# Kernel tuning notes

Hardware: AMD Instinct MI355X
Metric: run time of the kernel (lower is better)

The kernel has to match this reference:

```python
import jax, jax.numpy as jnp
import numpy as np

B, N, C, K, D, H = 4, 16384, 256, 16, 4, 512
EPS = 1e-5


def setup_inputs() -> dict:
    key = jax.random.key(0)
    ks = jax.random.split(key, 16)
    s = 0.05  # weight scale
    inp = {
        "x": jax.random.normal(ks[0], (B, N, C), jnp.float32),
        "knn": jax.random.randint(ks[1], (B, N, K), 0, N, jnp.int32),
        "lfp_w": jax.random.normal(ks[2], (D, C, C), jnp.float32) * s,
        "lfp_bn_w": jax.random.uniform(ks[3], (D, C), jnp.float32),
        "lfp_bn_b": jax.random.normal(ks[4], (D, C), jnp.float32) * s,
        "mlp0_w1": jax.random.normal(ks[5], (C, H), jnp.float32) * s,
        "mlp0_b1": jax.random.normal(ks[6], (H,), jnp.float32) * s,
        "mlp0_w2": jax.random.normal(ks[7], (H, C), jnp.float32) * s,
        "mlp0_bn_w": jax.random.uniform(ks[8], (C,), jnp.float32),
        "mlp0_bn_b": jax.random.normal(ks[9], (C,), jnp.float32) * s,
        "mlps_w1": jax.random.normal(ks[10], (D // 2, C, H), jnp.float32) * s,
        "mlps_b1": jax.random.normal(ks[11], (D // 2, H), jnp.float32) * s,
        "mlps_w2": jax.random.normal(ks[12], (D // 2, H, C), jnp.float32) * s,
        "mlps_bn_w": jax.random.uniform(ks[13], (D // 2, C), jnp.float32),
        "mlps_bn_b": jax.random.normal(ks[14], (D // 2, C), jnp.float32) * s,
    }
    return inp


def _bn(y, w, b):
    # BatchNorm1d over flattened (B*N) rows, biased variance, train-mode stats
    m = y.mean(axis=(0, 1))
    v = ((y - m) ** 2).mean(axis=(0, 1))
    return (y - m) * jax.lax.rsqrt(v + EPS) * w + b


def _mlp(y, w1, b1, w2, bw, bb):
    h = jax.nn.gelu(jnp.einsum("bnc,ch->bnh", y, w1) + b1, approximate=False)
    return _bn(jnp.einsum("bnh,hc->bnc", h, w2), bw, bb)


def _lfp(y, knn, w, bw, bb):
    p = jnp.einsum("bnc,cd->bnd", y, w)               # linear proj, no bias
    nb = jax.vmap(lambda pb, kb: pb[kb])(p, knn)      # [B,N,K,C] neighbor gather
    return _bn(nb.max(axis=2) - p, bw, bb)            # max over knn minus self


def reference(x, knn, lfp_w, lfp_bn_w, lfp_bn_b,
              mlp0_w1, mlp0_b1, mlp0_w2, mlp0_bn_w, mlp0_bn_b,
              mlps_w1, mlps_b1, mlps_w2, mlps_bn_w, mlps_bn_b):
    # Block.forward (eval: drop_path = identity)
    x = x + _mlp(x, mlp0_w1, mlp0_b1, mlp0_w2, mlp0_bn_w, mlp0_bn_b)
    depth = lfp_w.shape[0]
    for i in range(depth):
        x = x + _lfp(x, knn, lfp_w[i], lfp_bn_w[i], lfp_bn_b[i])
        if i % 2 == 1:
            j = i // 2
            x = x + _mlp(x, mlps_w1[j], mlps_b1[j], mlps_w2[j],
                         mlps_bn_w[j], mlps_bn_b[j])
    return x
```

## Files before the change

### kernel.cpp

```cpp
#include <hip/hip_runtime.h>
#include <hip/hip_bf16.h>

#define M_TOTAL 65536
#define NPTS    16384
#define CDIM    256
#define KNN     16
#define HDIM    512
#define CSTR    136

typedef __bf16 bf16x8 __attribute__((ext_vector_type(8)));
typedef float  f32x4  __attribute__((ext_vector_type(4)));

__device__ inline float b2f(unsigned u) {
    union { unsigned v; float f; } x; x.v = u << 16; return x.f;
}
__device__ inline unsigned short f2b(float f) {
    union { float f; unsigned u; } x; x.f = f;
    unsigned r = x.u + 0x7fffu + ((x.u >> 16) & 1u);
    return (unsigned short)(r >> 16);
}
__device__ inline void gload_lds16(const void* g, void* l) {
    __builtin_amdgcn_global_load_lds(
        (const __attribute__((address_space(1))) unsigned*)g,
        (__attribute__((address_space(3))) unsigned*)l, 16, 0, 0);
}
__device__ inline float gelu_tanh(float u) {
    const float t = u * (0.7978845608f + 0.0356774081f * u * u);
    const float e = __expf(2.f * t);
    const float th = 1.f - 2.f * __builtin_amdgcn_rcpf(e + 1.f);
    return 0.5f * u * (1.f + th);
}

template<int MODE>
__global__ __launch_bounds__(256) void gemm_nt(
    const short* __restrict__ A, const short* __restrict__ BT,
    short* __restrict__ outB,
    const float* __restrict__ bias, float2* __restrict__ partials,
    int N, int K)
{
    __shared__ short a_lds[128 * 32];
    __shared__ short b_lds[128 * 32];
    __shared__ short c_lds[128 * CSTR];
    __shared__ float s_sum[128], s_sq[128];

    const int tid = threadIdx.x;
    const int nx = gridDim.x, nwg = nx * gridDim.y;
    const int bid = blockIdx.y * nx + blockIdx.x;
    const int lid = (bid & 7) * (nwg >> 3) + (bid >> 3);
    const int m0 = (lid / nx) * 128, n0 = (lid % nx) * 128;

    const int w = tid >> 6, l = tid & 63;
    const int wm = w >> 1, wn = w & 1;

    if (MODE == 2 && tid < 128) { s_sum[tid] = 0.f; s_sq[tid] = 0.f; }

    f32x4 acc[4][4] = {};

    const int lrow = l & 15, lk = (l >> 4) * 8;
    const int q0 = 2 * w, q1 = 2 * w + 1;
    const int gr = l >> 2, gc = (l & 3) * 8;
    const size_t arow0 = (size_t)(m0 + q0 * 16 + gr) * K + gc;
    const size_t arow1 = (size_t)(m0 + q1 * 16 + gr) * K + gc;
    const size_t brow0 = (size_t)(n0 + q0 * 16 + gr) * K + gc;
    const size_t brow1 = (size_t)(n0 + q1 * 16 + gr) * K + gc;

    const int nkt = K >> 5;
    for (int kt = 0; kt < nkt; ++kt) {
        const int k0 = kt << 5;
        if (kt) __syncthreads();
        gload_lds16(A  + arow0 + k0, a_lds + q0 * 512);
        gload_lds16(A  + arow1 + k0, a_lds + q1 * 512);
        gload_lds16(BT + brow0 + k0, b_lds + q0 * 512);
        gload_lds16(BT + brow1 + k0, b_lds + q1 * 512);
        __syncthreads();

        bf16x8 af[4], bfr[4];
#pragma unroll
        for (int i = 0; i < 4; ++i)
            af[i] = *(const bf16x8*)(a_lds + (wm * 64 + i * 16 + lrow) * 32 + lk);
#pragma unroll
        for (int j = 0; j < 4; ++j)
            bfr[j] = *(const bf16x8*)(b_lds + (wn * 64 + j * 16 + lrow) * 32 + lk);
#pragma unroll
        for (int i = 0; i < 4; ++i)
#pragma unroll
            for (int j = 0; j < 4; ++j)
                acc[i][j] = __builtin_amdgcn_mfma_f32_16x16x32_bf16(
                    af[i], bfr[j], acc[i][j], 0, 0, 0);
    }

    const int lq = l >> 4;
#pragma unroll
    for (int j = 0; j < 4; ++j) {
        const int cl  = wn * 64 + j * 16 + lrow;
        const float bsv = (MODE == 1) ? bias[n0 + cl] : 0.f;
        float psum = 0.f, psq = 0.f;
#pragma unroll
        for (int i = 0; i < 4; ++i) {
#pragma unroll
            for (int r = 0; r < 4; ++r) {
                const int row = wm * 64 + i * 16 + lq * 4 + r;
                float v = acc[i][j][r];
                if (MODE == 1) v = gelu_tanh(v + bsv);
                c_lds[row * CSTR + cl] = (short)f2b(v);
                if (MODE == 2) { psum += v; psq += v * v; }
            }
        }
        if (MODE == 2) {
            atomicAdd(&s_sum[cl], psum);
            atomicAdd(&s_sq[cl], psq);
        }
    }
    __syncthreads();
#pragma unroll
    for (int it = 0; it < 8; ++it) {
        const int idx = it * 256 + tid;
        const int row = idx >> 4, ch = idx & 15;
        const uint4 vv = *(const uint4*)&c_lds[row * CSTR + ch * 8];
        *(uint4*)&outB[(size_t)(m0 + row) * N + n0 + ch * 8] = vv;
    }
    if (MODE == 2 && tid < 128)
        partials[(size_t)(m0 >> 7) * N + n0 + tid] =
            make_float2(s_sum[tid], s_sq[tid]);
}

__global__ __launch_bounds__(256) void gather_max(
    const short* __restrict__ p, const int* __restrict__ knn,
    short* __restrict__ yout, float2* __restrict__ partials, int pass)
{
    __shared__ float s_sum[128], s_sq[128];
    const int tid = threadIdx.x, w = tid >> 6, l = tid & 63;
    if (tid < 128) { s_sum[tid] = 0.f; s_sq[tid] = 0.f; }
    __syncthreads();

    const int xcd = blockIdx.x & 7, hi = blockIdx.x >> 3;
    const int gblk = (xcd >> 1) * 512 + (hi << 1) + (xcd & 1);

    const int sub = l >> 5;
    const int cl  = (l & 31) * 4;
    const int coff = pass * 128 + cl;

    float sa0 = 0, sa1 = 0, sa2 = 0, sa3 = 0;
    float qa0 = 0, qa1 = 0, qa2 = 0, qa3 = 0;
    for (int it = 0; it < 4; ++it) {
        const size_t g = (size_t)gblk * 32 + w * 8 + it * 2 + sub;
        const int b = (int)(g >> 14);
        const int n = (int)(g & (NPTS - 1));
        const int4* kp4 = (const int4*)(knn + ((size_t)b * NPTS + n) * KNN);
        int idxs[16];
        {
            const int4 i0 = kp4[0], i1 = kp4[1], i2 = kp4[2], i3 = kp4[3];
            idxs[0]=i0.x; idxs[1]=i0.y; idxs[2]=i0.z; idxs[3]=i0.w;
            idxs[4]=i1.x; idxs[5]=i1.y; idxs[6]=i1.z; idxs[7]=i1.w;
            idxs[8]=i2.x; idxs[9]=i2.y; idxs[10]=i2.z; idxs[11]=i2.w;
            idxs[12]=i3.x; idxs[13]=i3.y; idxs[14]=i3.z; idxs[15]=i3.w;
        }
        const size_t pbase = (size_t)b * NPTS * CDIM + coff;
        float mx0 = -1e30f, mx1 = -1e30f, mx2 = -1e30f, mx3 = -1e30f;
#pragma unroll
        for (int k = 0; k < KNN; ++k) {
            const uint2 v = *(const uint2*)(p + pbase + (size_t)idxs[k] * CDIM);
            mx0 = fmaxf(mx0, b2f(v.x & 0xffffu));
            mx1 = fmaxf(mx1, b2f(v.x >> 16));
            mx2 = fmaxf(mx2, b2f(v.y & 0xffffu));
            mx3 = fmaxf(mx3, b2f(v.y >> 16));
        }
        const uint2 sv = *(const uint2*)(p + g * CDIM + coff);
        const float t0 = mx0 - b2f(sv.x & 0xffffu);
        const float t1 = mx1 - b2f(sv.x >> 16);
        const float t2 = mx2 - b2f(sv.y & 0xffffu);
        const float t3 = mx3 - b2f(sv.y >> 16);
        uint2 pk;
        pk.x = (unsigned)f2b(t0) | ((unsigned)f2b(t1) << 16);
        pk.y = (unsigned)f2b(t2) | ((unsigned)f2b(t3) << 16);
        *(uint2*)(yout + g * CDIM + coff) = pk;
        sa0 += t0; sa1 += t1; sa2 += t2; sa3 += t3;
        qa0 += t0 * t0; qa1 += t1 * t1; qa2 += t2 * t2; qa3 += t3 * t3;
    }
    atomicAdd(&s_sum[cl + 0], sa0); atomicAdd(&s_sq[cl + 0], qa0);
    atomicAdd(&s_sum[cl + 1], sa1); atomicAdd(&s_sq[cl + 1], qa1);
    atomicAdd(&s_sum[cl + 2], sa2); atomicAdd(&s_sq[cl + 2], qa2);
    atomicAdd(&s_sum[cl + 3], sa3); atomicAdd(&s_sq[cl + 3], qa3);
    __syncthreads();
    if (tid < 128)
        partials[(size_t)gblk * CDIM + pass * 128 + tid] =
            make_float2(s_sum[tid], s_sq[tid]);
}

__global__ __launch_bounds__(256) void reduce_stats(
    const float2* __restrict__ partials, int nblk,
    const float* __restrict__ bnw, const float* __restrict__ bnb,
    float2* __restrict__ scsh)
{
    __shared__ float ss[4], qq[4];
    const int c = blockIdx.x;
    const int tid = threadIdx.x, w = tid >> 6, l = tid & 63;
    float s = 0.f, q = 0.f;
    for (int rb = tid; rb < nblk; rb += 256) {
        const float2 v = partials[(size_t)rb * CDIM + c];
        s += v.x; q += v.y;
    }
#pragma unroll
    for (int off = 32; off > 0; off >>= 1) {
        s += __shfl_down(s, off);
        q += __shfl_down(q, off);
    }
    if (l == 0) { ss[w] = s; qq[w] = q; }
    __syncthreads();
    if (tid == 0) {
        const float S = ss[0] + ss[1] + ss[2] + ss[3];
        const float Q = qq[0] + qq[1] + qq[2] + qq[3];
        const float invM = 1.f / 65536.f;
        const float mean = S * invM;
        const float var  = Q * invM - mean * mean;
        const float istd = rsqrtf(var + 1e-5f);
        const float sc   = bnw[c] * istd;
        scsh[c] = make_float2(sc, bnb[c] - mean * sc);
    }
}

__global__ __launch_bounds__(256) void bn_residual(
    const short* __restrict__ y, const float* __restrict__ resid,
    const float2* __restrict__ scsh,
    float* __restrict__ xout, short* __restrict__ xbout)
{
    const size_t t = (size_t)blockIdx.x * 256 + threadIdx.x;
    const uint2 yv = ((const uint2*)y)[t];
    const float4 rv = ((const float4*)resid)[t];
    const int c0 = (int)((t * 4) & (CDIM - 1));
    const float2 s0 = scsh[c0], s1 = scsh[c0 + 1], s2 = scsh[c0 + 2], s3 = scsh[c0 + 3];
    const float o0 = rv.x + b2f(yv.x & 0xffffu) * s0.x + s0.y;
    const float o1 = rv.y + b2f(yv.x >> 16)     * s1.x + s1.y;
    const float o2 = rv.z + b2f(yv.y & 0xffffu) * s2.x + s2.y;
    const float o3 = rv.w + b2f(yv.y >> 16)     * s3.x + s3.y;
    ((float4*)xout)[t] = make_float4(o0, o1, o2, o3);
    if (xbout) {
        uint2 pk;
        pk.x = (unsigned)f2b(o0) | ((unsigned)f2b(o1) << 16);
        pk.y = (unsigned)f2b(o2) | ((unsigned)f2b(o3) << 16);
        ((uint2*)xbout)[t] = pk;
    }
}

__global__ __launch_bounds__(256) void cast_x(
    const float* __restrict__ x, short* __restrict__ xb)
{
    const size_t t = (size_t)blockIdx.x * 256 + threadIdx.x;
    const float4 v = ((const float4*)x)[t];
    uint2 pk;
    pk.x = (unsigned)f2b(v.x) | ((unsigned)f2b(v.y) << 16);
    pk.y = (unsigned)f2b(v.z) | ((unsigned)f2b(v.w) << 16);
    ((uint2*)xb)[t] = pk;
}

__global__ __launch_bounds__(256) void transpose_cast(
    const float* __restrict__ src, short* __restrict__ dst, int R, int Cc)
{
    const size_t base = (size_t)blockIdx.y * R * Cc;
    const int i = blockIdx.x * 256 + threadIdx.x;
    if (i < R * Cc) {
        const int r = i / Cc, c = i % Cc;
        dst[base + (size_t)c * R + r] = (short)f2b(src[base + i]);
    }
}


extern "C" void kernel_launch(void* const* d_in, const int* in_sizes, int n_in,
                              void* d_out, int out_size, void* d_ws, size_t ws_size,
                              hipStream_t stream)
{
    (void)in_sizes; (void)n_in; (void)out_size; (void)ws_size;

    const float* x_in      = (const float*)d_in[0];
    const int*   knn       = (const int*)  d_in[1];
    const float* lfp_w     = (const float*)d_in[2];
    const float* lfp_bn_w  = (const float*)d_in[3];
    const float* lfp_bn_b  = (const float*)d_in[4];
    const float* mlp0_w1   = (const float*)d_in[5];
    const float* mlp0_b1   = (const float*)d_in[6];
    const float* mlp0_w2   = (const float*)d_in[7];
    const float* mlp0_bn_w = (const float*)d_in[8];
    const float* mlp0_bn_b = (const float*)d_in[9];
    const float* mlps_w1   = (const float*)d_in[10];
    const float* mlps_b1   = (const float*)d_in[11];
    const float* mlps_w2   = (const float*)d_in[12];
    const float* mlps_bn_w = (const float*)d_in[13];
    const float* mlps_bn_b = (const float*)d_in[14];

    char* ws = (char*)d_ws;
    short*  xb       = (short*) (ws + 0);
    short*  ybB      = (short*) (ws + 33554432ull);
    short*  hp       = (short*) (ws + 67108864ull);
    float2* partials = (float2*)(ws + 134217728ull);
    float2* scsh     = (float2*)(ws + 138412032ull);
    short*  lfpWT    = (short*) (ws + 138414080ull);
    short*  w1T0     = (short*) (ws + 138938368ull);
    short*  w2T0     = (short*) (ws + 139200512ull);
    short*  w1Ts     = (short*) (ws + 139462656ull);
    short*  w2Ts     = (short*) (ws + 139986944ull);
    float*  xout     = (float*)d_out;

    const dim3 blk(256);

    transpose_cast<<<dim3(256, 4), blk, 0, stream>>>(lfp_w,   lfpWT, 256, 256);
    transpose_cast<<<dim3(512, 1), blk, 0, stream>>>(mlp0_w1, w1T0,  256, 512);
    transpose_cast<<<dim3(512, 1), blk, 0, stream>>>(mlp0_w2, w2T0,  512, 256);
    transpose_cast<<<dim3(512, 2), blk, 0, stream>>>(mlps_w1, w1Ts,  256, 512);
    transpose_cast<<<dim3(512, 2), blk, 0, stream>>>(mlps_w2, w2Ts,  512, 256);
    cast_x<<<16384, blk, 0, stream>>>(x_in, xb);

    auto run_mlp = [&](const short* w1T, const float* b1, const short* w2T,
                       const float* bnw, const float* bnb, const float* resid,
                       bool last) {
        gemm_nt<1><<<dim3(4, 512), blk, 0, stream>>>(xb, w1T, hp,  b1, nullptr, 512, 256);
        gemm_nt<2><<<dim3(2, 512), blk, 0, stream>>>(hp, w2T, ybB, nullptr, partials, 256, 512);
        reduce_stats<<<256, blk, 0, stream>>>(partials, 512, bnw, bnb, scsh);
        bn_residual<<<16384, blk, 0, stream>>>(ybB, resid, scsh, xout, last ? nullptr : xb);
    };

    run_mlp(w1T0, mlp0_b1, w2T0, mlp0_bn_w, mlp0_bn_b, x_in, false);

    for (int i = 0; i < 4; ++i) {
        gemm_nt<0><<<dim3(2, 512), blk, 0, stream>>>(xb, lfpWT + (size_t)i * 65536,
                                                     hp, nullptr, nullptr, 256, 256);
        gather_max<<<2048, blk, 0, stream>>>(hp, knn, ybB, partials, 0);
        gather_max<<<2048, blk, 0, stream>>>(hp, knn, ybB, partials, 1);
        reduce_stats<<<256, blk, 0, stream>>>(partials, 2048,
                                              lfp_bn_w + i * 256, lfp_bn_b + i * 256, scsh);
        bn_residual<<<16384, blk, 0, stream>>>(ybB, xout, scsh, xout, xb);
        if (i & 1) {
            const int j = i >> 1;
            run_mlp(w1Ts + (size_t)j * 131072, mlps_b1 + j * 512,
                    w2Ts + (size_t)j * 131072,
                    mlps_bn_w + j * 256, mlps_bn_b + j * 256, xout,
                    i == 3);
        }
    }
}
```

Before: 952.7 us.

## Merge gather passes, keep residual in bf16, split stats reduction, widen vectors

gather_max now covers all 256 channels in a single launch, with each lane loading 16-byte vectors and all 16 neighbour loads issued before the max. The fp32 residual stream is replaced by the bf16 copy for the intermediate blocks, so bn_residual reads and writes bf16 and only the final step writes fp32, which removes a large amount of fp32 traffic per layer. The stats reduction becomes a two-stage, coalesced 16-block plus 1-block reduction, and bn_residual handles 8 elements per thread. Accumulating the residual in bf16 adds rounding error across layers and may break tolerance.

```diff
diff --git a/kernel.cpp b/kernel.cpp
--- a/kernel.cpp
+++ b/kernel.cpp
@@ -29,6 +29,12 @@
     const float e = __expf(2.f * t);
     const float th = 1.f - 2.f * __builtin_amdgcn_rcpf(e + 1.f);
     return 0.5f * u * (1.f + th);
+}
+__device__ inline void fmax8(uint4 v, float* mx) {
+    mx[0] = fmaxf(mx[0], b2f(v.x & 0xffffu)); mx[1] = fmaxf(mx[1], b2f(v.x >> 16));
+    mx[2] = fmaxf(mx[2], b2f(v.y & 0xffffu)); mx[3] = fmaxf(mx[3], b2f(v.y >> 16));
+    mx[4] = fmaxf(mx[4], b2f(v.z & 0xffffu)); mx[5] = fmaxf(mx[5], b2f(v.z >> 16));
+    mx[6] = fmaxf(mx[6], b2f(v.w & 0xffffu)); mx[7] = fmaxf(mx[7], b2f(v.w >> 16));
 }
 
 template<int MODE>
@@ -126,119 +132,140 @@
 
 __global__ __launch_bounds__(256) void gather_max(
     const short* __restrict__ p, const int* __restrict__ knn,
-    short* __restrict__ yout, float2* __restrict__ partials, int pass)
-{
-    __shared__ float s_sum[128], s_sq[128];
+    short* __restrict__ yout, float2* __restrict__ partials)
+{
+    __shared__ float s_sum[256], s_sq[256];
     const int tid = threadIdx.x, w = tid >> 6, l = tid & 63;
-    if (tid < 128) { s_sum[tid] = 0.f; s_sq[tid] = 0.f; }
+    s_sum[tid] = 0.f; s_sq[tid] = 0.f;
     __syncthreads();
 
     const int xcd = blockIdx.x & 7, hi = blockIdx.x >> 3;
     const int gblk = (xcd >> 1) * 512 + (hi << 1) + (xcd & 1);
 
     const int sub = l >> 5;
-    const int cl  = (l & 31) * 4;
-    const int coff = pass * 128 + cl;
-
-    float sa0 = 0, sa1 = 0, sa2 = 0, sa3 = 0;
-    float qa0 = 0, qa1 = 0, qa2 = 0, qa3 = 0;
+    const int cl8 = (l & 31) * 8;
+
+    float sa[8] = {}, qa[8] = {};
     for (int it = 0; it < 4; ++it) {
         const size_t g = (size_t)gblk * 32 + w * 8 + it * 2 + sub;
         const int b = (int)(g >> 14);
-        const int n = (int)(g & (NPTS - 1));
-        const int4* kp4 = (const int4*)(knn + ((size_t)b * NPTS + n) * KNN);
+        const int4* kp4 = (const int4*)(knn) + g * 4;
+        const int4 k0 = kp4[0], k1 = kp4[1], k2 = kp4[2], k3 = kp4[3];
         int idxs[16];
-        {
-            const int4 i0 = kp4[0], i1 = kp4[1], i2 = kp4[2], i3 = kp4[3];
-            idxs[0]=i0.x; idxs[1]=i0.y; idxs[2]=i0.z; idxs[3]=i0.w;
-            idxs[4]=i1.x; idxs[5]=i1.y; idxs[6]=i1.z; idxs[7]=i1.w;
-            idxs[8]=i2.x; idxs[9]=i2.y; idxs[10]=i2.z; idxs[11]=i2.w;
-            idxs[12]=i3.x; idxs[13]=i3.y; idxs[14]=i3.z; idxs[15]=i3.w;
-        }
-        const size_t pbase = (size_t)b * NPTS * CDIM + coff;
-        float mx0 = -1e30f, mx1 = -1e30f, mx2 = -1e30f, mx3 = -1e30f;
-#pragma unroll
-        for (int k = 0; k < KNN; ++k) {
-            const uint2 v = *(const uint2*)(p + pbase + (size_t)idxs[k] * CDIM);
-            mx0 = fmaxf(mx0, b2f(v.x & 0xffffu));
-            mx1 = fmaxf(mx1, b2f(v.x >> 16));
-            mx2 = fmaxf(mx2, b2f(v.y & 0xffffu));
-            mx3 = fmaxf(mx3, b2f(v.y >> 16));
-        }
-        const uint2 sv = *(const uint2*)(p + g * CDIM + coff);
-        const float t0 = mx0 - b2f(sv.x & 0xffffu);
-        const float t1 = mx1 - b2f(sv.x >> 16);
-        const float t2 = mx2 - b2f(sv.y & 0xffffu);
-        const float t3 = mx3 - b2f(sv.y >> 16);
-        uint2 pk;
-        pk.x = (unsigned)f2b(t0) | ((unsigned)f2b(t1) << 16);
-        pk.y = (unsigned)f2b(t2) | ((unsigned)f2b(t3) << 16);
-        *(uint2*)(yout + g * CDIM + coff) = pk;
-        sa0 += t0; sa1 += t1; sa2 += t2; sa3 += t3;
-        qa0 += t0 * t0; qa1 += t1 * t1; qa2 += t2 * t2; qa3 += t3 * t3;
-    }
-    atomicAdd(&s_sum[cl + 0], sa0); atomicAdd(&s_sq[cl + 0], qa0);
-    atomicAdd(&s_sum[cl + 1], sa1); atomicAdd(&s_sq[cl + 1], qa1);
-    atomicAdd(&s_sum[cl + 2], sa2); atomicAdd(&s_sq[cl + 2], qa2);
-    atomicAdd(&s_sum[cl + 3], sa3); atomicAdd(&s_sq[cl + 3], qa3);
+        idxs[0]=k0.x; idxs[1]=k0.y; idxs[2]=k0.z; idxs[3]=k0.w;
+        idxs[4]=k1.x; idxs[5]=k1.y; idxs[6]=k1.z; idxs[7]=k1.w;
+        idxs[8]=k2.x; idxs[9]=k2.y; idxs[10]=k2.z; idxs[11]=k2.w;
+        idxs[12]=k3.x; idxs[13]=k3.y; idxs[14]=k3.z; idxs[15]=k3.w;
+        const short* pb = p + (size_t)b * NPTS * CDIM + cl8;
+        uint4 v[16];
+#pragma unroll
+        for (int k = 0; k < 16; ++k)
+            v[k] = *(const uint4*)(pb + (size_t)idxs[k] * CDIM);
+        const uint4 sv = *(const uint4*)(p + g * CDIM + cl8);
+
+        float mx[8] = {-1e30f,-1e30f,-1e30f,-1e30f,-1e30f,-1e30f,-1e30f,-1e30f};
+#pragma unroll
+        for (int k = 0; k < 16; ++k) fmax8(v[k], mx);
+
+        float t[8];
+        t[0] = mx[0] - b2f(sv.x & 0xffffu); t[1] = mx[1] - b2f(sv.x >> 16);
+        t[2] = mx[2] - b2f(sv.y & 0xffffu); t[3] = mx[3] - b2f(sv.y >> 16);
+        t[4] = mx[4] - b2f(sv.z & 0xffffu); t[5] = mx[5] - b2f(sv.z >> 16);
+        t[6] = mx[6] - b2f(sv.w & 0xffffu); t[7] = mx[7] - b2f(sv.w >> 16);
+
+        uint4 pk;
+        pk.x = (unsigned)f2b(t[0]) | ((unsigned)f2b(t[1]) << 16);
+        pk.y = (unsigned)f2b(t[2]) | ((unsigned)f2b(t[3]) << 16);
+        pk.z = (unsigned)f2b(t[4]) | ((unsigned)f2b(t[5]) << 16);
+        pk.w = (unsigned)f2b(t[6]) | ((unsigned)f2b(t[7]) << 16);
+        *(uint4*)(yout + g * CDIM + cl8) = pk;
+#pragma unroll
+        for (int j = 0; j < 8; ++j) { sa[j] += t[j]; qa[j] += t[j] * t[j]; }
+    }
+#pragma unroll
+    for (int j = 0; j < 8; ++j) {
+        atomicAdd(&s_sum[cl8 + j], sa[j]);
+        atomicAdd(&s_sq[cl8 + j], qa[j]);
+    }
     __syncthreads();
-    if (tid < 128)
-        partials[(size_t)gblk * CDIM + pass * 128 + tid] =
-            make_float2(s_sum[tid], s_sq[tid]);
-}
-
-__global__ __launch_bounds__(256) void reduce_stats(
-    const float2* __restrict__ partials, int nblk,
+    partials[(size_t)gblk * CDIM + tid] = make_float2(s_sum[tid], s_sq[tid]);
+}
+
+__global__ __launch_bounds__(256) void reduce_stats1(
+    const float2* __restrict__ partials, int nblk, float2* __restrict__ part2)
+{
+    const int tid = threadIdx.x;
+    float s = 0.f, q = 0.f;
+    for (int rb = blockIdx.x; rb < nblk; rb += 16) {
+        const float2 v = partials[(size_t)rb * CDIM + tid];
+        s += v.x; q += v.y;
+    }
+    part2[(size_t)blockIdx.x * CDIM + tid] = make_float2(s, q);
+}
+__global__ __launch_bounds__(256) void reduce_stats2(
+    const float2* __restrict__ part2,
     const float* __restrict__ bnw, const float* __restrict__ bnb,
     float2* __restrict__ scsh)
 {
-    __shared__ float ss[4], qq[4];
-    const int c = blockIdx.x;
-    const int tid = threadIdx.x, w = tid >> 6, l = tid & 63;
+    const int c = threadIdx.x;
     float s = 0.f, q = 0.f;
-    for (int rb = tid; rb < nblk; rb += 256) {
-        const float2 v = partials[(size_t)rb * CDIM + c];
+#pragma unroll
+    for (int b = 0; b < 16; ++b) {
+        const float2 v = part2[(size_t)b * CDIM + c];
         s += v.x; q += v.y;
     }
-#pragma unroll
-    for (int off = 32; off > 0; off >>= 1) {
-        s += __shfl_down(s, off);
-        q += __shfl_down(q, off);
-    }
-    if (l == 0) { ss[w] = s; qq[w] = q; }
-    __syncthreads();
-    if (tid == 0) {
-        const float S = ss[0] + ss[1] + ss[2] + ss[3];
-        const float Q = qq[0] + qq[1] + qq[2] + qq[3];
-        const float invM = 1.f / 65536.f;
-        const float mean = S * invM;
-        const float var  = Q * invM - mean * mean;
-        const float istd = rsqrtf(var + 1e-5f);
-        const float sc   = bnw[c] * istd;
-        scsh[c] = make_float2(sc, bnb[c] - mean * sc);
-    }
-}
-
+    const float invM = 1.f / 65536.f;
+    const float mean = s * invM;
+    const float var  = q * invM - mean * mean;
+    const float istd = rsqrtf(var + 1e-5f);
+    const float sc   = bnw[c] * istd;
+    scsh[c] = make_float2(sc, bnb[c] - mean * sc);
+}
+
+template<int V>
 __global__ __launch_bounds__(256) void bn_residual(
-    const short* __restrict__ y, const float* __restrict__ resid,
-    const float2* __restrict__ scsh,
-    float* __restrict__ xout, short* __restrict__ xbout)
+    const short* __restrict__ y, const short* __restrict__ xb_in,
+    const float* __restrict__ xf_in, const float2* __restrict__ scsh,
+    short* __restrict__ xb_out, float* __restrict__ xf_out)
 {
     const size_t t = (size_t)blockIdx.x * 256 + threadIdx.x;
-    const uint2 yv = ((const uint2*)y)[t];
-    const float4 rv = ((const float4*)resid)[t];
-    const int c0 = (int)((t * 4) & (CDIM - 1));
-    const float2 s0 = scsh[c0], s1 = scsh[c0 + 1], s2 = scsh[c0 + 2], s3 = scsh[c0 + 3];
-    const float o0 = rv.x + b2f(yv.x & 0xffffu) * s0.x + s0.y;
-    const float o1 = rv.y + b2f(yv.x >> 16)     * s1.x + s1.y;
-    const float o2 = rv.z + b2f(yv.y & 0xffffu) * s2.x + s2.y;
-    const float o3 = rv.w + b2f(yv.y >> 16)     * s3.x + s3.y;
-    ((float4*)xout)[t] = make_float4(o0, o1, o2, o3);
-    if (xbout) {
-        uint2 pk;
-        pk.x = (unsigned)f2b(o0) | ((unsigned)f2b(o1) << 16);
-        pk.y = (unsigned)f2b(o2) | ((unsigned)f2b(o3) << 16);
-        ((uint2*)xbout)[t] = pk;
+    const uint4 yv = ((const uint4*)y)[t];
+    float xr[8];
+    if (V == 1) {
+        const float4 a = ((const float4*)xf_in)[2 * t];
+        const float4 b = ((const float4*)xf_in)[2 * t + 1];
+        xr[0]=a.x; xr[1]=a.y; xr[2]=a.z; xr[3]=a.w;
+        xr[4]=b.x; xr[5]=b.y; xr[6]=b.z; xr[7]=b.w;
+    } else {
+        const uint4 xv = ((const uint4*)xb_in)[t];
+        xr[0]=b2f(xv.x & 0xffffu); xr[1]=b2f(xv.x >> 16);
+        xr[2]=b2f(xv.y & 0xffffu); xr[3]=b2f(xv.y >> 16);
+        xr[4]=b2f(xv.z & 0xffffu); xr[5]=b2f(xv.z >> 16);
+        xr[6]=b2f(xv.w & 0xffffu); xr[7]=b2f(xv.w >> 16);
+    }
+    float yr[8];
+    yr[0]=b2f(yv.x & 0xffffu); yr[1]=b2f(yv.x >> 16);
+    yr[2]=b2f(yv.y & 0xffffu); yr[3]=b2f(yv.y >> 16);
+    yr[4]=b2f(yv.z & 0xffffu); yr[5]=b2f(yv.z >> 16);
+    yr[6]=b2f(yv.w & 0xffffu); yr[7]=b2f(yv.w >> 16);
+
+    const int c0 = (int)((t * 8) & (CDIM - 1));
+    float o[8];
+#pragma unroll
+    for (int j = 0; j < 8; ++j) {
+        const float2 sc = scsh[c0 + j];
+        o[j] = xr[j] + yr[j] * sc.x + sc.y;
+    }
+    if (V == 2) {
+        ((float4*)xf_out)[2 * t]     = make_float4(o[0], o[1], o[2], o[3]);
+        ((float4*)xf_out)[2 * t + 1] = make_float4(o[4], o[5], o[6], o[7]);
+    } else {
+        uint4 pk;
+        pk.x = (unsigned)f2b(o[0]) | ((unsigned)f2b(o[1]) << 16);
+        pk.y = (unsigned)f2b(o[2]) | ((unsigned)f2b(o[3]) << 16);
+        pk.z = (unsigned)f2b(o[4]) | ((unsigned)f2b(o[5]) << 16);
+        pk.w = (unsigned)f2b(o[6]) | ((unsigned)f2b(o[7]) << 16);
+        ((uint4*)xb_out)[t] = pk;
     }
 }
 
@@ -292,12 +319,13 @@
     short*  ybB      = (short*) (ws + 33554432ull);
     short*  hp       = (short*) (ws + 67108864ull);
     float2* partials = (float2*)(ws + 134217728ull);
-    float2* scsh     = (float2*)(ws + 138412032ull);
-    short*  lfpWT    = (short*) (ws + 138414080ull);
-    short*  w1T0     = (short*) (ws + 138938368ull);
-    short*  w2T0     = (short*) (ws + 139200512ull);
-    short*  w1Ts     = (short*) (ws + 139462656ull);
-    short*  w2Ts     = (short*) (ws + 139986944ull);
+    float2* part2    = (float2*)(ws + 138412032ull);
+    float2* scsh     = (float2*)(ws + 138444800ull);
+    short*  lfpWT    = (short*) (ws + 138446848ull);
+    short*  w1T0     = (short*) (ws + 138971136ull);
+    short*  w2T0     = (short*) (ws + 139233280ull);
+    short*  w1Ts     = (short*) (ws + 139495424ull);
+    short*  w2Ts     = (short*) (ws + 140019712ull);
     float*  xout     = (float*)d_out;
 
     const dim3 blk(256);
@@ -309,31 +337,38 @@
     transpose_cast<<<dim3(512, 2), blk, 0, stream>>>(mlps_w2, w2Ts,  512, 256);
     cast_x<<<16384, blk, 0, stream>>>(x_in, xb);
 
+    auto run_stats = [&](int nblk, const float* bnw, const float* bnb) {
+        reduce_stats1<<<16, blk, 0, stream>>>(partials, nblk, part2);
+        reduce_stats2<<<1, blk, 0, stream>>>(part2, bnw, bnb, scsh);
+    };
+
     auto run_mlp = [&](const short* w1T, const float* b1, const short* w2T,
-                       const float* bnw, const float* bnb, const float* resid,
-                       bool last) {
+                       const float* bnw, const float* bnb, int variant) {
         gemm_nt<1><<<dim3(4, 512), blk, 0, stream>>>(xb, w1T, hp,  b1, nullptr, 512, 256);
         gemm_nt<2><<<dim3(2, 512), blk, 0, stream>>>(hp, w2T, ybB, nullptr, partials, 256, 512);
-        reduce_stats<<<256, blk, 0, stream>>>(partials, 512, bnw, bnb, scsh);
-        bn_residual<<<16384, blk, 0, stream>>>(ybB, resid, scsh, xout, last ? nullptr : xb);
+        run_stats(512, bnw, bnb);
+        if (variant == 1)
+            bn_residual<1><<<8192, blk, 0, stream>>>(ybB, nullptr, x_in, scsh, xb, nullptr);
+        else if (variant == 2)
+            bn_residual<2><<<8192, blk, 0, stream>>>(ybB, xb, nullptr, scsh, nullptr, xout);
+        else
+            bn_residual<0><<<8192, blk, 0, stream>>>(ybB, xb, nullptr, scsh, xb, nullptr);
     };
 
-    run_mlp(w1T0, mlp0_b1, w2T0, mlp0_bn_w, mlp0_bn_b, x_in, false);
+    run_mlp(w1T0, mlp0_b1, w2T0, mlp0_bn_w, mlp0_bn_b, 1);
 
     for (int i = 0; i < 4; ++i) {
         gemm_nt<0><<<dim3(2, 512), blk, 0, stream>>>(xb, lfpWT + (size_t)i * 65536,
                                                      hp, nullptr, nullptr, 256, 256);
-        gather_max<<<2048, blk, 0, stream>>>(hp, knn, ybB, partials, 0);
-        gather_max<<<2048, blk, 0, stream>>>(hp, knn, ybB, partials, 1);
-        reduce_stats<<<256, blk, 0, stream>>>(partials, 2048,
-                                              lfp_bn_w + i * 256, lfp_bn_b + i * 256, scsh);
-        bn_residual<<<16384, blk, 0, stream>>>(ybB, xout, scsh, xout, xb);
+        gather_max<<<2048, blk, 0, stream>>>(hp, knn, ybB, partials);
+        run_stats(2048, lfp_bn_w + i * 256, lfp_bn_b + i * 256);
+        bn_residual<0><<<8192, blk, 0, stream>>>(ybB, xb, nullptr, scsh, xb, nullptr);
         if (i & 1) {
             const int j = i >> 1;
             run_mlp(w1Ts + (size_t)j * 131072, mlps_b1 + j * 512,
                     w2Ts + (size_t)j * 131072,
-                    mlps_bn_w + j * 256, mlps_bn_b + j * 256, xout,
-                    i == 3);
+                    mlps_bn_w + j * 256, mlps_bn_b + j * 256,
+                    (i == 3) ? 2 : 0);
         }
     }
 }
```

Result: faster. 932.1 us (-2.2%).
